# Kernel optimization log

Hardware: AMD Instinct MI355X
Metric: run time of the kernel (lower is better)

## Reference

```python
import jax, jax.numpy as jnp
import numpy as np

B, S, D, H = 4, 2048, 1024, 16
HD = D // H  # 64


def setup_inputs() -> dict:
    key = jax.random.key(0)
    ks = jax.random.split(key, 11)
    scale = 1.0 / np.sqrt(D)
    inp = {
        "query": jax.random.normal(ks[0], (B, S, D), jnp.float32),
        "key": jax.random.normal(ks[1], (B, S, D), jnp.float32),
        "value": jax.random.normal(ks[2], (B, S, D), jnp.float32),
        "mask": jnp.ones((B, 1, 1, S), jnp.float32),
        "wq": jax.random.normal(ks[3], (D, D), jnp.float32) * scale,
        "bq": jnp.zeros((D,), jnp.float32),
        "wk": jax.random.normal(ks[4], (D, D), jnp.float32) * scale,
        "bk": jnp.zeros((D,), jnp.float32),
        "wv": jax.random.normal(ks[5], (D, D), jnp.float32) * scale,
        "bv": jnp.zeros((D,), jnp.float32),
        "wo": jax.random.normal(ks[6], (D, D), jnp.float32) * scale,
        "bo": jnp.zeros((D,), jnp.float32),
    }
    return inp


def reference(query, key, value, mask, wq, bq, wk, bk, wv, bv, wo, bo):
    b = query.shape[0]
    # Dense QKV projections
    q = query @ wq + bq  # [B,S,D]
    k = key @ wk + bk
    v = value @ wv + bv

    def split_heads(x):
        return x.reshape(b, -1, H, HD).transpose(0, 2, 1, 3)  # [B,H,S,HD]

    q, k, v = split_heads(q), split_heads(k), split_heads(v)
    score = jnp.einsum("bhqd,bhkd->bhqk", q, k) / jnp.sqrt(jnp.float32(HD))
    score = score + (1.0 - mask) * -1e9
    alpha = jax.nn.softmax(score, axis=-1)
    context = jnp.einsum("bhqk,bhkd->bhqd", alpha, v)  # [B,H,S,HD]
    context = context.transpose(0, 2, 1, 3).reshape(b, -1, D)
    return context @ wo + bo
```

## Files before the change

kernel.cpp:

```cpp
#include <hip/hip_runtime.h>

using u16 = unsigned short;
using u32 = unsigned int;

typedef float  f32x4  __attribute__((ext_vector_type(4)));
typedef float  f32x16 __attribute__((ext_vector_type(16)));
typedef u32    u32x4  __attribute__((ext_vector_type(4)));
typedef _Float16 f16;
typedef f16 f16x8 __attribute__((ext_vector_type(8)));

#define DEVI static __device__ __forceinline__

constexpr int S_  = 2048;
constexpr int D_  = 1024;
constexpr int HD_ = 64;
constexpr int SH_ = S_*HD_;
constexpr size_t NE_ = 8192ull*1024ull;

DEVI f32x4 mfma16f(f16x8 a, f16x8 b, f32x4 c){
  return __builtin_amdgcn_mfma_f32_16x16x32_f16(a, b, c, 0, 0, 0);
}
DEVI f32x16 mfma32(f16x8 a, f16x8 b, f32x16 c){
  return __builtin_amdgcn_mfma_f32_32x32x16_f16(a, b, c, 0, 0, 0);
}
DEVI float exp2fast(float x){
#if __has_builtin(__builtin_amdgcn_exp2f)
  return __builtin_amdgcn_exp2f(x);
#else
  float r; asm("v_exp_f32 %0, %1" : "=v"(r) : "v"(x)); return r;
#endif
}
DEVI float rcpfast(float x){
#if __has_builtin(__builtin_amdgcn_rcpf)
  return __builtin_amdgcn_rcpf(x);
#else
  float r; asm("v_rcp_f32 %0, %1" : "=v"(r) : "v"(x)); return r;
#endif
}
DEVI u32 pkh(float a, float b){
  return __builtin_bit_cast(u32, __builtin_amdgcn_cvt_pkrtz(a, b));
}
DEVI void gld16(const void* g, void* l){
  __builtin_amdgcn_global_load_lds(
      (const __attribute__((address_space(1))) u32*)g,
      (__attribute__((address_space(3))) u32*)l, 16, 0, 0);
}
DEVI void gld4(const void* g, void* l){
  __builtin_amdgcn_global_load_lds(
      (const __attribute__((address_space(1))) u32*)g,
      (__attribute__((address_space(3))) u32*)l, 4, 0, 0);
}

__global__ __launch_bounds__(256) void wcvt_k(
    const float* __restrict__ wq, const float* __restrict__ wk,
    const float* __restrict__ wv, const float* __restrict__ wo,
    u16* __restrict__ wt)
{
  int z = blockIdx.z;
  const float* W = (z==0)?wq:(z==1)?wk:(z==2)?wv:wo;
  u16* ot = wt + (size_t)z*D_*D_;
  __shared__ float t[64][65];
  int k0 = blockIdx.y*64, n0 = blockIdx.x*64;
  int tid = threadIdx.x;
#pragma unroll
  for (int i=0;i<4;i++){
    int lin = i*256 + tid;
    int r = lin>>4, c = (lin&15)*4;
    f32x4 v = *reinterpret_cast<const f32x4*>(W + (size_t)(k0+r)*D_ + n0 + c);
    t[r][c+0]=v.x; t[r][c+1]=v.y; t[r][c+2]=v.z; t[r][c+3]=v.w;
  }
  __syncthreads();
  int n = tid>>2, c0 = (tid&3)*16;
  alignas(16) u16 hb[16];
#pragma unroll
  for (int i=0;i<16;i++) hb[i] = __builtin_bit_cast(u16, (f16)t[c0+i][n]);
  size_t off = (size_t)(n0+n)*D_ + k0 + c0;
  *reinterpret_cast<u32x4*>(ot+off)   = *reinterpret_cast<u32x4*>(hb);
  *reinterpret_cast<u32x4*>(ot+off+8) = *reinterpret_cast<u32x4*>(hb+8);
}

__global__ __launch_bounds__(256) void madd_k(const float* __restrict__ mask,
                                              float* __restrict__ madd2)
{
  int i = blockIdx.x*256 + threadIdx.x;
  if (i < 4*S_) madd2[i] = (1.0f - mask[i]) * -1442695040.0f;
}

struct GemmArgs {
  const void* A[3];
  const u16*  Wt[3];
  const float* bias[3];
  float*      outF[3];
  u16*        outH[3];
  float       scale[3];
  int         mode[3];
};

template<bool AF32>
__global__ __launch_bounds__(256) void gemm_k(GemmArgs args)
{
  int z = blockIdx.z;
  const float* __restrict__ Af  = (const float*)args.A[z];
  const u16*   __restrict__ Ah  = (const u16*)args.A[z];
  const u16*   __restrict__ Wt  = args.Wt[z];
  const float* __restrict__ bias = args.bias[z];
  int mode = args.mode[z];
  float sc = args.scale[z];

  constexpr int ABYT = AF32 ? 16384 : 8192;
  constexpr int BUFS = ABYT + 8192;
  __shared__ __align__(16) unsigned char smem[AF32 ? 73728 : 49152];
  char* sbase = (char*)smem;

  int m0 = blockIdx.x*128, n0 = blockIdx.y*128;
  int tid = threadIdx.x, lane = tid&63, w = tid>>6;
  int wm = (w>>1)*64, wn = (w&1)*64;
  int lr = lane&15, lh = lane>>4;

  int offA[AF32?4:2], offB[2];
  if constexpr (AF32){
#pragma unroll
    for (int j=0;j<4;j++){
      int chunk = w*4 + j;
      int row = chunk*8 + (lane>>3);
      int g = lane&7;
      offA[j] = row*D_ + ((g ^ (row&7))*4);
    }
  } else {
#pragma unroll
    for (int j=0;j<2;j++){
      int chunk = w*2 + j;
      int row = chunk*16 + (lane>>2);
      int gs = lane&3;
      offA[j] = row*D_ + ((gs ^ (row&3))*8);
    }
  }
#pragma unroll
  for (int j=0;j<2;j++){
    int chunk = w*2 + j;
    int row = chunk*16 + (lane>>2);
    int gs = lane&3;
    offB[j] = row*D_ + ((gs ^ (row&3))*8);
  }

  f32x4 acc[4][4];
#pragma unroll
  for (int m=0;m<4;m++)
#pragma unroll
    for (int n=0;n<4;n++) acc[m][n] = f32x4{0.f,0.f,0.f,0.f};

  auto STAGE = [&](int buf, int kt){
    char* lA = sbase + buf*BUFS;
    char* lB = lA + ABYT;
    if constexpr (AF32){
      const float* As = Af + (size_t)m0*D_ + kt*32;
#pragma unroll
      for (int j=0;j<4;j++) gld16(As + offA[j], lA + (w*4+j)*1024);
    } else {
      const u16* As = Ah + (size_t)m0*D_ + kt*32;
#pragma unroll
      for (int j=0;j<2;j++) gld16(As + offA[j], lA + (w*2+j)*1024);
    }
    const u16* Bs = Wt + (size_t)n0*D_ + kt*32;
#pragma unroll
    for (int j=0;j<2;j++) gld16(Bs + offB[j], lB + (w*2+j)*1024);
  };

  STAGE(0, 0);
  STAGE(1, 1);
  STAGE(2, 2);

  for (int kt=0; kt<32; ++kt){
    int buf = kt - (kt/3)*3;
    if (kt < 30){
      if constexpr (AF32) asm volatile("s_waitcnt vmcnt(12)" ::: "memory");
      else                asm volatile("s_waitcnt vmcnt(8)"  ::: "memory");
    } else if (kt == 30){
      if constexpr (AF32) asm volatile("s_waitcnt vmcnt(6)" ::: "memory");
      else                asm volatile("s_waitcnt vmcnt(4)" ::: "memory");
    } else {
      asm volatile("s_waitcnt vmcnt(0)" ::: "memory");
    }
    __builtin_amdgcn_s_barrier();

    char* bA = sbase + buf*BUFS;
    char* bB = bA + ABYT;
    f16x8 af[4], bfr[4];
#pragma unroll
    for (int m=0;m<4;m++){
      int row = wm + m*16 + lr;
      if constexpr (AF32){
        f32x4 a0 = *reinterpret_cast<const f32x4*>(bA + row*128 + ((((lh<<1)  ) ^ (row&7))<<4));
        f32x4 a1 = *reinterpret_cast<const f32x4*>(bA + row*128 + ((((lh<<1)|1) ^ (row&7))<<4));
        u32x4 uw;
        uw.x = pkh(a0.x,a0.y); uw.y = pkh(a0.z,a0.w);
        uw.z = pkh(a1.x,a1.y); uw.w = pkh(a1.z,a1.w);
        af[m] = __builtin_bit_cast(f16x8, uw);
      } else {
        af[m] = *reinterpret_cast<const f16x8*>(bA + ((row*64 + lh*16) ^ ((row&3)<<4)));
      }
    }
#pragma unroll
    for (int n=0;n<4;n++){
      int row = wn + n*16 + lr;
      bfr[n] = *reinterpret_cast<const f16x8*>(bB + ((row*64 + lh*16) ^ ((row&3)<<4)));
    }
    asm volatile("s_waitcnt lgkmcnt(0)" ::: "memory");
    __builtin_amdgcn_sched_barrier(0);
    __builtin_amdgcn_s_barrier();
    if (kt < 29) STAGE(buf, kt+3);

    __builtin_amdgcn_s_setprio(1);
#pragma unroll
    for (int m=0;m<4;m++)
#pragma unroll
      for (int n=0;n<4;n++)
        acc[m][n] = mfma16f(af[m], bfr[n], acc[m][n]);
    __builtin_amdgcn_s_setprio(0);
  }

  float bsetv[4];
#pragma unroll
  for (int n=0;n<4;n++) bsetv[n] = bias[n0 + wn + n*16 + lr];

  if (mode == 0){
    float* out = args.outF[z];
#pragma unroll
    for (int m=0;m<4;m++)
#pragma unroll
      for (int n=0;n<4;n++)
#pragma unroll
        for (int r=0;r<4;r++){
          int row = m0 + wm + m*16 + lh*4 + r;
          int col = n0 + wn + n*16 + lr;
          out[(size_t)row*D_ + col] = (acc[m][n][r] + bsetv[n])*sc;
        }
  } else if (mode == 1){
    u16* oh = args.outH[z];
#pragma unroll
    for (int m=0;m<4;m++)
#pragma unroll
      for (int n=0;n<4;n++)
#pragma unroll
        for (int r=0;r<4;r++){
          int row = m0 + wm + m*16 + lh*4 + r;
          int col = n0 + wn + n*16 + lr;
          float val = (acc[m][n][r] + bsetv[n])*sc;
          int b = row >> 11, s = row & 2047;
          int hh = col >> 6,  dd = col & 63;
          oh[(size_t)(b*16 + hh)*SH_ + (size_t)s*HD_ + dd] =
              __builtin_bit_cast(u16, (f16)val);
        }
  } else {
    __syncthreads();
    u16* ct = (u16*)sbase;
#pragma unroll
    for (int m=0;m<4;m++)
#pragma unroll
      for (int n=0;n<4;n++)
#pragma unroll
        for (int r=0;r<4;r++){
          int lrow = wm + m*16 + lh*4 + r;
          int lcol = wn + n*16 + lr;
          ct[lrow*132 + lcol] = __builtin_bit_cast(u16, (f16)((acc[m][n][r] + bsetv[n])*sc));
        }
    __syncthreads();
    u16* ovt = args.outH[z];
    int b = m0 >> 11, s0 = m0 & 2047;
    int ch = tid >> 1, half = tid & 1;
    int gn = n0 + ch;
    int hh = gn >> 6, dd = gn & 63;
    size_t obase = (size_t)(b*16 + hh)*SH_ + (size_t)dd*S_ + s0 + half*64;
#pragma unroll
    for (int i=0;i<8;i++){
      alignas(16) u16 tmp[8];
#pragma unroll
      for (int j=0;j<8;j++) tmp[j] = ct[(half*64 + i*8 + j)*132 + ch];
      *reinterpret_cast<u32x4*>(ovt + obase + i*8) = *reinterpret_cast<u32x4*>(tmp);
    }
  }
}

__global__ __launch_bounds__(256) void attn_k(
    const f16* __restrict__ Qf, const f16* __restrict__ Kf,
    const f16* __restrict__ Vt, const float* __restrict__ madd2,
    u16* __restrict__ cf)
{
  __shared__ __align__(16) unsigned char smem[33280];
  char* sbase = (char*)smem;

  int flat = blockIdx.x + blockIdx.y*gridDim.x;
  int xcd = flat & 7, ix = flat >> 3;
  int bh = xcd + 8*(ix >> 4);
  int qx = ix & 15;
  int b = bh >> 4, head = bh & 15;

  const f16* Qb = Qf + (size_t)bh*SH_;
  const f16* Kb = Kf + (size_t)bh*SH_;
  const f16* Vb = Vt + (size_t)bh*SH_;
  const float* mb = madd2 + (size_t)b*S_;

  int tid = threadIdx.x, lane = tid&63, w = tid>>6;
  int q31 = lane&31, h = lane>>5;
  int qw = qx*128 + w*32;
  int xorv = (q31&7)<<4;

  f16x8 qb[4];
#pragma unroll
  for (int ks=0;ks<4;ks++)
    qb[ks] = *reinterpret_cast<const f16x8*>(Qb + (size_t)(qw + q31)*HD_ + ks*16 + h*8);

  int offK[2], offV[2];
#pragma unroll
  for (int j=0;j<2;j++){
    int L = (w*2+j)*1024 + lane*16;
    int r = L>>7;
    int dby = (L&127) ^ ((r&7)<<4);
    offK[j] = r*HD_ + (dby>>1);
    offV[j] = r*S_  + (dby>>1);
  }

  u32 one2 = 0x3C003C00u;
  u32x4 onev; onev.x=one2; onev.y=one2; onev.z=one2; onev.w=one2;
  f16x8 vones = __builtin_bit_cast(f16x8, onev);

  f32x16 o[2], ol;
#pragma unroll
  for (int n=0;n<2;n++)
#pragma unroll
    for (int r=0;r<16;r++) o[n][r] = 0.f;
#pragma unroll
  for (int r=0;r<16;r++) ol[r] = 0.f;

  auto STAGE = [&](int buf, int kt){
    int kv0 = kt*64;
    char* sKb = sbase + buf*8192;
    char* sVb = sbase + 16384 + buf*8192;
    char* sMb = sbase + 32768 + buf*256;
#pragma unroll
    for (int j=0;j<2;j++)
      gld16(Kb + (size_t)kv0*HD_ + offK[j], sKb + (w*2+j)*1024);
#pragma unroll
    for (int j=0;j<2;j++)
      gld16(Vb + kv0 + offV[j], sVb + (w*2+j)*1024);
    gld4(mb + kv0 + lane, sMb);
  };

  STAGE(0, 0);

  for (int kt=0; kt<32; ++kt){
    int buf = kt&1;
    char* sKb = sbase + buf*8192;
    char* sVb = sbase + 16384 + buf*8192;
    float* sMb = (float*)(sbase + 32768 + buf*256);

    asm volatile("s_waitcnt vmcnt(0)" ::: "memory");
    __builtin_amdgcn_s_barrier();
    if (kt < 31) STAGE(buf^1, kt+1);

    f32x16 st[2];
#pragma unroll
    for (int n=0;n<2;n++)
#pragma unroll
      for (int r=0;r<16;r++) st[n][r] = 0.f;

    __builtin_amdgcn_s_setprio(1);
#pragma unroll
    for (int n=0;n<2;n++){
      int rb = (n*32 + q31)*128;
#pragma unroll
      for (int ks=0;ks<4;ks++){
        f16x8 ka = *reinterpret_cast<const f16x8*>(sKb + ((rb + ks*32 + h*16) ^ xorv));
        st[n] = mfma32(ka, qb[ks], st[n]);
      }
    }
    __builtin_amdgcn_s_setprio(0);

    float mval = sMb[lane];
    if (__ballot(mval != 0.0f)){
#pragma unroll
      for (int n=0;n<2;n++)
#pragma unroll
        for (int g=0;g<4;g++){
          f32x4 mv = *reinterpret_cast<const f32x4*>(sMb + n*32 + g*8 + h*4);
#pragma unroll
          for (int c=0;c<4;c++) st[n][g*4+c] += mv[c];
        }
    }

#pragma unroll
    for (int n=0;n<2;n++)
#pragma unroll
      for (int r=0;r<16;r++) st[n][r] = exp2fast(st[n][r]);

    f16x8 pa[4];
#pragma unroll
    for (int n=0;n<2;n++){
      u32 x[4], y[4];
#pragma unroll
      for (int T=0;T<4;T++){
        x[T] = pkh(st[n][4*T+0], st[n][4*T+1]);
        y[T] = pkh(st[n][4*T+2], st[n][4*T+3]);
      }
#pragma unroll
      for (int k2=0;k2<2;k2++){
        u32 a0=x[2*k2], b0=x[2*k2+1], a1=y[2*k2], b1=y[2*k2+1];
        asm volatile("v_permlane32_swap_b32 %0, %1" : "+v"(a0), "+v"(b0));
        asm volatile("v_permlane32_swap_b32 %0, %1" : "+v"(a1), "+v"(b1));
        u32x4 wv;
        wv.x = a0;
        wv.y = a1;
        wv.z = b0;
        wv.w = b1;
        pa[2*n+k2] = __builtin_bit_cast(f16x8, wv);
      }
    }

    __builtin_amdgcn_s_setprio(1);
#pragma unroll
    for (int n=0;n<2;n++){
      int rb = (n*32 + q31)*128;
#pragma unroll
      for (int ks=0;ks<4;ks++){
        f16x8 vbf = *reinterpret_cast<const f16x8*>(sVb + ((rb + ks*32 + h*16) ^ xorv));
        o[n] = mfma32(pa[ks], vbf, o[n]);
      }
    }
#pragma unroll
    for (int ks=0;ks<4;ks++)
      ol = mfma32(pa[ks], vones, ol);
    __builtin_amdgcn_s_setprio(0);
  }

#pragma unroll
  for (int n=0;n<2;n++)
#pragma unroll
    for (int r=0;r<16;r++){
      float inv = rcpfast(ol[r]);
      int s = qw + (r&3) + 8*(r>>2) + 4*h;
      int d = head*HD_ + n*32 + q31;
      cf[((size_t)(b*S_ + s))*D_ + d] = __builtin_bit_cast(u16, (f16)(o[n][r]*inv));
    }
}

extern "C" void kernel_launch(void* const* d_in, const int* in_sizes, int n_in,
                              void* d_out, int out_size, void* d_ws, size_t ws_size,
                              hipStream_t stream)
{
  (void)in_sizes; (void)n_in; (void)out_size;
  const float* query=(const float*)d_in[0];
  const float* key  =(const float*)d_in[1];
  const float* value=(const float*)d_in[2];
  const float* mask =(const float*)d_in[3];
  const float* wq=(const float*)d_in[4];
  const float* bq=(const float*)d_in[5];
  const float* wk=(const float*)d_in[6];
  const float* bk=(const float*)d_in[7];
  const float* wv=(const float*)d_in[8];
  const float* bv=(const float*)d_in[9];
  const float* wo=(const float*)d_in[10];
  const float* bo=(const float*)d_in[11];
  float* out = (float*)d_out;

  const size_t WN = 4ull*1024*1024;
  size_t need = WN*2 + 4*NE_*2 + 8192*4;
  if (ws_size < need) return;

  char* ws = (char*)d_ws;
  u16* wt = (u16*)ws;
  u16* qf = wt + WN;
  u16* kf = qf + NE_;
  u16* vt = kf + NE_;
  u16* cf = vt + NE_;
  float* madd2 = (float*)(cf + NE_);

  const float CSC = 0.18033688011112042f;

  wcvt_k<<<dim3(16,16,4), 256, 0, stream>>>(wq,wk,wv,wo,wt);
  madd_k<<<dim3(32), 256, 0, stream>>>(mask, madd2);

  GemmArgs ga{};
  ga.A[0]=query; ga.A[1]=key; ga.A[2]=value;
  ga.Wt[0]=wt;           ga.Wt[1]=wt+1048576;   ga.Wt[2]=wt+2097152;
  ga.bias[0]=bq; ga.bias[1]=bk; ga.bias[2]=bv;
  ga.scale[0]=CSC; ga.scale[1]=1.0f; ga.scale[2]=1.0f;
  ga.mode[0]=1;  ga.mode[1]=1;  ga.mode[2]=2;
  ga.outH[0]=qf; ga.outH[1]=kf; ga.outH[2]=vt;
  gemm_k<true><<<dim3(64,8,3), 256, 0, stream>>>(ga);

  attn_k<<<dim3(16,64), 256, 0, stream>>>((const f16*)qf,(const f16*)kf,(const f16*)vt,madd2,cf);

  GemmArgs go{};
  go.A[0]=cf;
  go.Wt[0]=wt+3145728;
  go.bias[0]=bo; go.scale[0]=1.0f; go.mode[0]=0; go.outF[0]=out;
  gemm_k<false><<<dim3(64,8,1), 256, 0, stream>>>(go);
}
```

Baseline: 219.9 us.

## Pre-convert activations to fp16 and use 256x128 GEMM tiles with 512 threads

```diff
diff --git a/kernel.cpp b/kernel.cpp
--- a/kernel.cpp
+++ b/kernel.cpp
@@ -77,6 +77,22 @@
   size_t off = (size_t)(n0+n)*D_ + k0 + c0;
   *reinterpret_cast<u32x4*>(ot+off)   = *reinterpret_cast<u32x4*>(hb);
   *reinterpret_cast<u32x4*>(ot+off+8) = *reinterpret_cast<u32x4*>(hb+8);
+}
+
+__global__ __launch_bounds__(256) void acvt_k(
+    const float* __restrict__ q, const float* __restrict__ k,
+    const float* __restrict__ v, u16* __restrict__ out)
+{
+  int z = blockIdx.y;
+  const float* src = (z==0)?q:(z==1)?k:v;
+  u16* dst = out + (size_t)z*NE_;
+  size_t i = ((size_t)blockIdx.x*256 + threadIdx.x)*8;
+  f32x4 a = *reinterpret_cast<const f32x4*>(src + i);
+  f32x4 b = *reinterpret_cast<const f32x4*>(src + i + 4);
+  u32x4 t;
+  t.x = pkh(a.x,a.y); t.y = pkh(a.z,a.w);
+  t.z = pkh(b.x,b.y); t.w = pkh(b.z,b.w);
+  *reinterpret_cast<u32x4*>(dst + i) = t;
 }
 
 __global__ __launch_bounds__(256) void madd_k(const float* __restrict__ mask,
@@ -96,51 +112,37 @@
   int         mode[3];
 };
 
-template<bool AF32>
-__global__ __launch_bounds__(256) void gemm_k(GemmArgs args)
+__global__ __launch_bounds__(512, 4) void gemm_k(GemmArgs args)
 {
   int z = blockIdx.z;
-  const float* __restrict__ Af  = (const float*)args.A[z];
-  const u16*   __restrict__ Ah  = (const u16*)args.A[z];
-  const u16*   __restrict__ Wt  = args.Wt[z];
+  const u16*   __restrict__ A    = (const u16*)args.A[z];
+  const u16*   __restrict__ Wt   = args.Wt[z];
   const float* __restrict__ bias = args.bias[z];
   int mode = args.mode[z];
   float sc = args.scale[z];
 
-  constexpr int ABYT = AF32 ? 16384 : 8192;
+  constexpr int ABYT = 16384;
   constexpr int BUFS = ABYT + 8192;
-  __shared__ __align__(16) unsigned char smem[AF32 ? 73728 : 49152];
+  __shared__ __align__(16) unsigned char smem[73728];
   char* sbase = (char*)smem;
 
-  int m0 = blockIdx.x*128, n0 = blockIdx.y*128;
+  int m0 = blockIdx.x*256, n0 = blockIdx.y*128;
   int tid = threadIdx.x, lane = tid&63, w = tid>>6;
   int wm = (w>>1)*64, wn = (w&1)*64;
   int lr = lane&15, lh = lane>>4;
 
-  int offA[AF32?4:2], offB[2];
-  if constexpr (AF32){
-#pragma unroll
-    for (int j=0;j<4;j++){
-      int chunk = w*4 + j;
-      int row = chunk*8 + (lane>>3);
-      int g = lane&7;
-      offA[j] = row*D_ + ((g ^ (row&7))*4);
-    }
-  } else {
-#pragma unroll
-    for (int j=0;j<2;j++){
-      int chunk = w*2 + j;
-      int row = chunk*16 + (lane>>2);
-      int gs = lane&3;
-      offA[j] = row*D_ + ((gs ^ (row&3))*8);
-    }
-  }
+  int offA[2], offB;
 #pragma unroll
   for (int j=0;j<2;j++){
     int chunk = w*2 + j;
     int row = chunk*16 + (lane>>2);
     int gs = lane&3;
-    offB[j] = row*D_ + ((gs ^ (row&3))*8);
+    offA[j] = row*D_ + (((gs - (row>>1)) & 3)*8);
+  }
+  {
+    int row = w*16 + (lane>>2);
+    int gs = lane&3;
+    offB = row*D_ + (((gs - (row>>1)) & 3)*8);
   }
 
   f32x4 acc[4][4];
@@ -152,18 +154,11 @@
   auto STAGE = [&](int buf, int kt){
     char* lA = sbase + buf*BUFS;
     char* lB = lA + ABYT;
-    if constexpr (AF32){
-      const float* As = Af + (size_t)m0*D_ + kt*32;
-#pragma unroll
-      for (int j=0;j<4;j++) gld16(As + offA[j], lA + (w*4+j)*1024);
-    } else {
-      const u16* As = Ah + (size_t)m0*D_ + kt*32;
-#pragma unroll
-      for (int j=0;j<2;j++) gld16(As + offA[j], lA + (w*2+j)*1024);
-    }
+    const u16* As = A  + (size_t)m0*D_ + kt*32;
+#pragma unroll
+    for (int j=0;j<2;j++) gld16(As + offA[j], lA + (w*2+j)*1024);
     const u16* Bs = Wt + (size_t)n0*D_ + kt*32;
-#pragma unroll
-    for (int j=0;j<2;j++) gld16(Bs + offB[j], lB + (w*2+j)*1024);
+    gld16(Bs + offB, lB + w*1024);
   };
 
   STAGE(0, 0);
@@ -172,15 +167,9 @@
 
   for (int kt=0; kt<32; ++kt){
     int buf = kt - (kt/3)*3;
-    if (kt < 30){
-      if constexpr (AF32) asm volatile("s_waitcnt vmcnt(12)" ::: "memory");
-      else                asm volatile("s_waitcnt vmcnt(8)"  ::: "memory");
-    } else if (kt == 30){
-      if constexpr (AF32) asm volatile("s_waitcnt vmcnt(6)" ::: "memory");
-      else                asm volatile("s_waitcnt vmcnt(4)" ::: "memory");
-    } else {
-      asm volatile("s_waitcnt vmcnt(0)" ::: "memory");
-    }
+    if (kt < 30)       asm volatile("s_waitcnt vmcnt(6)" ::: "memory");
+    else if (kt == 30) asm volatile("s_waitcnt vmcnt(3)" ::: "memory");
+    else               asm volatile("s_waitcnt vmcnt(0)" ::: "memory");
     __builtin_amdgcn_s_barrier();
 
     char* bA = sbase + buf*BUFS;
@@ -189,21 +178,12 @@
 #pragma unroll
     for (int m=0;m<4;m++){
       int row = wm + m*16 + lr;
-      if constexpr (AF32){
-        f32x4 a0 = *reinterpret_cast<const f32x4*>(bA + row*128 + ((((lh<<1)  ) ^ (row&7))<<4));
-        f32x4 a1 = *reinterpret_cast<const f32x4*>(bA + row*128 + ((((lh<<1)|1) ^ (row&7))<<4));
-        u32x4 uw;
-        uw.x = pkh(a0.x,a0.y); uw.y = pkh(a0.z,a0.w);
-        uw.z = pkh(a1.x,a1.y); uw.w = pkh(a1.z,a1.w);
-        af[m] = __builtin_bit_cast(f16x8, uw);
-      } else {
-        af[m] = *reinterpret_cast<const f16x8*>(bA + ((row*64 + lh*16) ^ ((row&3)<<4)));
-      }
+      af[m] = *reinterpret_cast<const f16x8*>(bA + row*64 + (((lh + (row>>1)) & 3)<<4));
     }
 #pragma unroll
     for (int n=0;n<4;n++){
       int row = wn + n*16 + lr;
-      bfr[n] = *reinterpret_cast<const f16x8*>(bB + ((row*64 + lh*16) ^ ((row&3)<<4)));
+      bfr[n] = *reinterpret_cast<const f16x8*>(bB + row*64 + (((lh + (row>>1)) & 3)<<4));
     }
     asm volatile("s_waitcnt lgkmcnt(0)" ::: "memory");
     __builtin_amdgcn_sched_barrier(0);
@@ -267,15 +247,15 @@
     __syncthreads();
     u16* ovt = args.outH[z];
     int b = m0 >> 11, s0 = m0 & 2047;
-    int ch = tid >> 1, half = tid & 1;
+    int ch = tid >> 2, quarter = tid & 3;
     int gn = n0 + ch;
     int hh = gn >> 6, dd = gn & 63;
-    size_t obase = (size_t)(b*16 + hh)*SH_ + (size_t)dd*S_ + s0 + half*64;
+    size_t obase = (size_t)(b*16 + hh)*SH_ + (size_t)dd*S_ + s0 + quarter*64;
 #pragma unroll
     for (int i=0;i<8;i++){
       alignas(16) u16 tmp[8];
 #pragma unroll
-      for (int j=0;j<8;j++) tmp[j] = ct[(half*64 + i*8 + j)*132 + ch];
+      for (int j=0;j<8;j++) tmp[j] = ct[(quarter*64 + i*8 + j)*132 + ch];
       *reinterpret_cast<u32x4*>(ovt + obase + i*8) = *reinterpret_cast<u32x4*>(tmp);
     }
   }
@@ -463,12 +443,15 @@
   float* out = (float*)d_out;
 
   const size_t WN = 4ull*1024*1024;
-  size_t need = WN*2 + 4*NE_*2 + 8192*4;
+  size_t need = WN*2 + 3*NE_*2 + 3*NE_*2 + NE_*2 + 8192*4;
   if (ws_size < need) return;
 
   char* ws = (char*)d_ws;
   u16* wt = (u16*)ws;
-  u16* qf = wt + WN;
+  u16* aq = wt + WN;
+  u16* ak = aq + NE_;
+  u16* av = ak + NE_;
+  u16* qf = av + NE_;
   u16* kf = qf + NE_;
   u16* vt = kf + NE_;
   u16* cf = vt + NE_;
@@ -477,16 +460,17 @@
   const float CSC = 0.18033688011112042f;
 
   wcvt_k<<<dim3(16,16,4), 256, 0, stream>>>(wq,wk,wv,wo,wt);
+  acvt_k<<<dim3(4096,3), 256, 0, stream>>>(query,key,value,aq);
   madd_k<<<dim3(32), 256, 0, stream>>>(mask, madd2);
 
   GemmArgs ga{};
-  ga.A[0]=query; ga.A[1]=key; ga.A[2]=value;
+  ga.A[0]=aq; ga.A[1]=ak; ga.A[2]=av;
   ga.Wt[0]=wt;           ga.Wt[1]=wt+1048576;   ga.Wt[2]=wt+2097152;
   ga.bias[0]=bq; ga.bias[1]=bk; ga.bias[2]=bv;
   ga.scale[0]=CSC; ga.scale[1]=1.0f; ga.scale[2]=1.0f;
   ga.mode[0]=1;  ga.mode[1]=1;  ga.mode[2]=2;
   ga.outH[0]=qf; ga.outH[1]=kf; ga.outH[2]=vt;
-  gemm_k<true><<<dim3(64,8,3), 256, 0, stream>>>(ga);
+  gemm_k<<<dim3(32,8,3), 512, 0, stream>>>(ga);
 
   attn_k<<<dim3(16,64), 256, 0, stream>>>((const f16*)qf,(const f16*)kf,(const f16*)vt,madd2,cf);
 
@@ -494,5 +478,5 @@
   go.A[0]=cf;
   go.Wt[0]=wt+3145728;
   go.bias[0]=bo; go.scale[0]=1.0f; go.mode[0]=0; go.outF[0]=out;
-  gemm_k<false><<<dim3(64,8,1), 256, 0, stream>>>(go);
-}
+  gemm_k<<<dim3(32,8,1), 512, 0, stream>>>(go);
+}
```

After: 224.8 us. +2.2%, slower.
